# Kernel optimization log

Measured on AMD Instinct MI355X. Metric: run time of the kernel, lower is better.

## Reference

```python
import jax, jax.numpy as jnp
import numpy as np

ALPHA = 50.0
BETA = 0.5
EPS = 1e-6

def setup_inputs() -> dict:
    key = jax.random.key(0)
    k1, k2, k3 = jax.random.split(key, 3)
    N, D = 131072, 512
    output1 = jax.random.normal(k1, (N, D), dtype=jnp.float32)
    output2 = jax.random.normal(k2, (N, D), dtype=jnp.float32)
    target = jax.random.randint(k3, (N,), 0, 2, dtype=jnp.int64)
    return {"output1": output1, "output2": output2, "target": target}

def reference(output1, output2, target):
    # per-pair cosine similarity (torch.nn.CosineSimilarity, dim=1, eps=1e-6)
    dot = jnp.sum(output1 * output2, axis=1)
    denom = jnp.maximum(jnp.linalg.norm(output1, axis=1) * jnp.linalg.norm(output2, axis=1), EPS)
    d = dot / denom  # [N]
    # binomial deviance terms
    pos = (2.0 / BETA) * jax.nn.softplus(-BETA * (d - 0.5))
    neg = (2.0 / ALPHA) * jax.nn.softplus(ALPHA * (d - 2.0))
    is_pos = (target == 1)
    num_pos = jnp.sum(is_pos)
    num_neg = target.shape[0] - num_pos
    pos_loss = jnp.sum(jnp.where(is_pos, pos, 0.0)) / jnp.maximum(num_pos, 1)
    neg_loss = jnp.sum(jnp.where(is_pos, 0.0, neg)) / jnp.maximum(num_neg, 1)
    return pos_loss + neg_loss
```

## Files before the change

### kernel.cpp

```cpp
#include <hip/hip_runtime.h>
#include <math.h>

#define N_ROWS 131072
#define D 512
#define BLOCKS 2048
#define WPB 4
#define NWAVES (BLOCKS * WPB)
#define RPW (N_ROWS / NWAVES)
#define EPS 1e-6f

#define WAIT_VM(N) __builtin_amdgcn_s_waitcnt(0x0F70 | ((N) & 0xF) | ((((N) >> 4) & 3) << 14))
#define PIN() __builtin_amdgcn_sched_barrier(0)

__device__ __forceinline__ float softplusf(float x) {
    return fmaxf(x, 0.0f) + log1pf(__expf(-fabsf(x)));
}

struct Slot { float4 a0, a1, b0, b1; };

#define ISSUE(S, T) do {                                        \
    const float* _p1 = pRow1 + (size_t)(T) * D;                 \
    const float* _p2 = pRow2 + (size_t)(T) * D;                 \
    S.a0 = *(const float4*)(_p1);                               \
    S.a1 = *(const float4*)(_p1 + 256);                         \
    S.b0 = *(const float4*)(_p2);                               \
    S.b1 = *(const float4*)(_p2 + 256);                         \
} while (0)

__device__ __forceinline__ void proc_tile(const Slot& s, int t, int lane,
                                          float& myDot, float& myS1, float& myS2) {
    float dot = s.a0.x * s.b0.x + s.a0.y * s.b0.y + s.a0.z * s.b0.z + s.a0.w * s.b0.w
              + s.a1.x * s.b1.x + s.a1.y * s.b1.y + s.a1.z * s.b1.z + s.a1.w * s.b1.w;
    float s1  = s.a0.x * s.a0.x + s.a0.y * s.a0.y + s.a0.z * s.a0.z + s.a0.w * s.a0.w
              + s.a1.x * s.a1.x + s.a1.y * s.a1.y + s.a1.z * s.a1.z + s.a1.w * s.a1.w;
    float s2  = s.b0.x * s.b0.x + s.b0.y * s.b0.y + s.b0.z * s.b0.z + s.b0.w * s.b0.w
              + s.b1.x * s.b1.x + s.b1.y * s.b1.y + s.b1.z * s.b1.z + s.b1.w * s.b1.w;
    #pragma unroll
    for (int off = 32; off > 0; off >>= 1) {
        dot += __shfl_xor(dot, off);
        s1  += __shfl_xor(s1, off);
        s2  += __shfl_xor(s2, off);
    }
    if (lane == t) { myDot = dot; myS1 = s1; myS2 = s2; }
}

#define STEP(SI, TI, SP, TP) do {                                \
    ISSUE(SI, TI); PIN(); WAIT_VM(12); PIN();                    \
    proc_tile(SP, TP, lane, myDot, myS1, myS2);                  \
} while (0)

__global__ __launch_bounds__(256, 4) void binloss_main(
    const float* __restrict__ o1, const float* __restrict__ o2,
    const int* __restrict__ target,
    float* __restrict__ sums, int* __restrict__ icnt,
    unsigned int* __restrict__ done, float* __restrict__ out) {

    __shared__ float sPos[WPB], sNeg[WPB];
    __shared__ int sCnt[WPB];

    const int lane = threadIdx.x & 63;
    const int wave = threadIdx.x >> 6;
    const int gwave = blockIdx.x * WPB + wave;
    const int rowBase = gwave * RPW;

    const int myT = target[rowBase + (lane & (RPW - 1))];

    const float* pRow1 = o1 + (size_t)rowBase * D + lane * 4;
    const float* pRow2 = o2 + (size_t)rowBase * D + lane * 4;

    float myDot = 0.0f, myS1 = 1.0f, myS2 = 1.0f;

    Slot s0, s1_, s2_, s3;

    ISSUE(s0, 0);
    ISSUE(s1_, 1);
    ISSUE(s2_, 2);

    STEP(s3, 3,  s0, 0);
    STEP(s0, 4,  s1_, 1);
    STEP(s1_, 5, s2_, 2);
    STEP(s2_, 6, s3, 3);
    STEP(s3, 7,  s0, 4);
    STEP(s0, 8,  s1_, 5);
    STEP(s1_, 9, s2_, 6);
    STEP(s2_, 10, s3, 7);
    STEP(s3, 11, s0, 8);
    STEP(s0, 12, s1_, 9);
    STEP(s1_, 13, s2_, 10);
    STEP(s2_, 14, s3, 11);
    STEP(s3, 15, s0, 12);
    WAIT_VM(8);  PIN(); proc_tile(s1_, 13, lane, myDot, myS1, myS2);
    WAIT_VM(4);  PIN(); proc_tile(s2_, 14, lane, myDot, myS1, myS2);
    WAIT_VM(0);  PIN(); proc_tile(s3, 15, lane, myDot, myS1, myS2);

    float d = myDot / fmaxf(sqrtf(myS1) * sqrtf(myS2), EPS);
    float posv = 0.0f, negv = 0.0f;
    int pc = 0;
    if (lane < RPW) {
        if (myT == 1) { posv = 4.0f * softplusf(-0.5f * (d - 0.5f)); pc = 1; }
        else          { negv = 0.04f * softplusf(50.0f * (d - 2.0f)); }
    }

    #pragma unroll
    for (int off = 32; off > 0; off >>= 1) {
        posv += __shfl_xor(posv, off);
        negv += __shfl_xor(negv, off);
        pc   += __shfl_xor(pc, off);
    }

    if (lane == 0) { sPos[wave] = posv; sNeg[wave] = negv; sCnt[wave] = pc; }
    __syncthreads();
    if (threadIdx.x == 0) {
        float p = sPos[0] + sPos[1] + sPos[2] + sPos[3];
        float n = sNeg[0] + sNeg[1] + sNeg[2] + sNeg[3];
        int c = sCnt[0] + sCnt[1] + sCnt[2] + sCnt[3];
        atomicAdd(&sums[0], p);
        atomicAdd(&sums[1], n);
        atomicAdd(&icnt[0], c);
        __threadfence();
        unsigned int old = atomicAdd(done, 1u);
        if (old == (unsigned int)(gridDim.x - 1)) {
            __threadfence();
            float ps = __hip_atomic_load(&sums[0], __ATOMIC_RELAXED, __HIP_MEMORY_SCOPE_AGENT);
            float ns = __hip_atomic_load(&sums[1], __ATOMIC_RELAXED, __HIP_MEMORY_SCOPE_AGENT);
            int np = __hip_atomic_load(&icnt[0], __ATOMIC_RELAXED, __HIP_MEMORY_SCOPE_AGENT);
            int nn = N_ROWS - np;
            out[0] = ps / (float)(np > 1 ? np : 1) + ns / (float)(nn > 1 ? nn : 1);
        }
    }
}

extern "C" void kernel_launch(void* const* d_in, const int* in_sizes, int n_in,
                              void* d_out, int out_size, void* d_ws, size_t ws_size,
                              hipStream_t stream) {
    const float* o1 = (const float*)d_in[0];
    const float* o2 = (const float*)d_in[1];
    const int* tgt = (const int*)d_in[2];
    float* out = (float*)d_out;
    float* sums = (float*)d_ws;
    int* cnt = (int*)((char*)d_ws + 8);
    unsigned int* done = (unsigned int*)((char*)d_ws + 12);

    hipMemsetAsync(d_ws, 0, 16, stream);
    binloss_main<<<BLOCKS, 256, 0, stream>>>(o1, o2, tgt, sums, cnt, done, out);
}
```

Measured before the change: 604.6 us.

## Interleave rows across waves and shrink prefetch depth to double buffering

Result: slower. 642.3 us (+6.2%).

```diff
diff --git a/kernel.cpp b/kernel.cpp
--- a/kernel.cpp
+++ b/kernel.cpp
@@ -6,7 +6,7 @@
 #define BLOCKS 2048
 #define WPB 4
 #define NWAVES (BLOCKS * WPB)
-#define RPW (N_ROWS / NWAVES)
+#define STEPS (N_ROWS / NWAVES)
 #define EPS 1e-6f
 
 #define WAIT_VM(N) __builtin_amdgcn_s_waitcnt(0x0F70 | ((N) & 0xF) | ((((N) >> 4) & 3) << 14))
@@ -18,16 +18,16 @@
 
 struct Slot { float4 a0, a1, b0, b1; };
 
-#define ISSUE(S, T) do {                                        \
-    const float* _p1 = pRow1 + (size_t)(T) * D;                 \
-    const float* _p2 = pRow2 + (size_t)(T) * D;                 \
-    S.a0 = *(const float4*)(_p1);                               \
-    S.a1 = *(const float4*)(_p1 + 256);                         \
-    S.b0 = *(const float4*)(_p2);                               \
-    S.b1 = *(const float4*)(_p2 + 256);                         \
+#define ISSUE(S, K) do {                                          \
+    const float* _p1 = pRow1 + (size_t)(K) * ((size_t)NWAVES * D);\
+    const float* _p2 = pRow2 + (size_t)(K) * ((size_t)NWAVES * D);\
+    S.a0 = *(const float4*)(_p1);                                 \
+    S.a1 = *(const float4*)(_p1 + 256);                           \
+    S.b0 = *(const float4*)(_p2);                                 \
+    S.b1 = *(const float4*)(_p2 + 256);                           \
 } while (0)
 
-__device__ __forceinline__ void proc_tile(const Slot& s, int t, int lane,
+__device__ __forceinline__ void proc_tile(const Slot& s, int k, int lane,
                                           float& myDot, float& myS1, float& myS2) {
     float dot = s.a0.x * s.b0.x + s.a0.y * s.b0.y + s.a0.z * s.b0.z + s.a0.w * s.b0.w
               + s.a1.x * s.b1.x + s.a1.y * s.b1.y + s.a1.z * s.b1.z + s.a1.w * s.b1.w;
@@ -41,15 +41,10 @@
         s1  += __shfl_xor(s1, off);
         s2  += __shfl_xor(s2, off);
     }
-    if (lane == t) { myDot = dot; myS1 = s1; myS2 = s2; }
+    if (lane == k) { myDot = dot; myS1 = s1; myS2 = s2; }
 }
 
-#define STEP(SI, TI, SP, TP) do {                                \
-    ISSUE(SI, TI); PIN(); WAIT_VM(12); PIN();                    \
-    proc_tile(SP, TP, lane, myDot, myS1, myS2);                  \
-} while (0)
-
-__global__ __launch_bounds__(256, 4) void binloss_main(
+__global__ __launch_bounds__(256, 8) void binloss_main(
     const float* __restrict__ o1, const float* __restrict__ o2,
     const int* __restrict__ target,
     float* __restrict__ sums, int* __restrict__ icnt,
@@ -61,42 +56,33 @@
     const int lane = threadIdx.x & 63;
     const int wave = threadIdx.x >> 6;
     const int gwave = blockIdx.x * WPB + wave;
-    const int rowBase = gwave * RPW;
 
-    const int myT = target[rowBase + (lane & (RPW - 1))];
-
-    const float* pRow1 = o1 + (size_t)rowBase * D + lane * 4;
-    const float* pRow2 = o2 + (size_t)rowBase * D + lane * 4;
+    const float* pRow1 = o1 + (size_t)gwave * D + lane * 4;
+    const float* pRow2 = o2 + (size_t)gwave * D + lane * 4;
 
     float myDot = 0.0f, myS1 = 1.0f, myS2 = 1.0f;
 
-    Slot s0, s1_, s2_, s3;
+    Slot sA, sB;
 
-    ISSUE(s0, 0);
-    ISSUE(s1_, 1);
-    ISSUE(s2_, 2);
+    ISSUE(sA, 0);
+    #pragma unroll
+    for (int k = 0; k < STEPS; k += 2) {
+        if (k + 1 < STEPS) { ISSUE(sB, k + 1); PIN(); WAIT_VM(4); PIN(); }
+        else               { PIN(); WAIT_VM(0); PIN(); }
+        proc_tile(sA, k, lane, myDot, myS1, myS2);
 
-    STEP(s3, 3,  s0, 0);
-    STEP(s0, 4,  s1_, 1);
-    STEP(s1_, 5, s2_, 2);
-    STEP(s2_, 6, s3, 3);
-    STEP(s3, 7,  s0, 4);
-    STEP(s0, 8,  s1_, 5);
-    STEP(s1_, 9, s2_, 6);
-    STEP(s2_, 10, s3, 7);
-    STEP(s3, 11, s0, 8);
-    STEP(s0, 12, s1_, 9);
-    STEP(s1_, 13, s2_, 10);
-    STEP(s2_, 14, s3, 11);
-    STEP(s3, 15, s0, 12);
-    WAIT_VM(8);  PIN(); proc_tile(s1_, 13, lane, myDot, myS1, myS2);
-    WAIT_VM(4);  PIN(); proc_tile(s2_, 14, lane, myDot, myS1, myS2);
-    WAIT_VM(0);  PIN(); proc_tile(s3, 15, lane, myDot, myS1, myS2);
+        if (k + 2 < STEPS) { ISSUE(sA, k + 2); PIN(); WAIT_VM(4); PIN(); }
+        else               { PIN(); WAIT_VM(0); PIN(); }
+        proc_tile(sB, k + 1, lane, myDot, myS1, myS2);
+    }
+
+    int myT = 0;
+    if (lane < STEPS) myT = target[gwave + lane * NWAVES];
 
     float d = myDot / fmaxf(sqrtf(myS1) * sqrtf(myS2), EPS);
     float posv = 0.0f, negv = 0.0f;
     int pc = 0;
-    if (lane < RPW) {
+    if (lane < STEPS) {
         if (myT == 1) { posv = 4.0f * softplusf(-0.5f * (d - 0.5f)); pc = 1; }
         else          { negv = 0.04f * softplusf(50.0f * (d - 2.0f)); }
     }
```
